# Optimization experiments

Hardware: AMD Instinct MI355X
Metric: run time of the kernel (lower is better)

The kernel has to match this reference:

```python
import jax, jax.numpy as jnp
import numpy as np

BATCH, IN, HID, OUT = 8192, 784, 4096, 10


def setup_inputs() -> dict:
    key = jax.random.key(0)
    k_x, k_w1, k_b1, k_w2, k_b2 = jax.random.split(key, 5)
    return {
        "x": jax.random.normal(k_x, (BATCH, IN), dtype=jnp.float32),
        "W1": jax.random.normal(k_w1, (HID, IN), dtype=jnp.float32) * 0.05,
        "b1": jax.random.normal(k_b1, (HID,), dtype=jnp.float32) * 0.05,
        "W2": jax.random.normal(k_w2, (OUT, HID), dtype=jnp.float32) * 0.05,
        "b2": jax.random.normal(k_b2, (OUT,), dtype=jnp.float32) * 0.05,
    }


def reference(x, W1, b1, W2, b2):
    # x: [B, 784] -- first layer, so the input is NOT binarized (BNN convention
    # for in_features == 784); only the weight is sign-quantized.
    x = x.reshape(-1, IN)
    Wb1 = jnp.sign(W1)                       # binarized weights in {-1, 0, +1}
    h = jnp.einsum("bi,hi->bh", x, Wb1) + b1  # BinarizeLinear fc1
    h = jnp.clip(h, -1.0, 1.0)               # Hardtanh
    out = jnp.einsum("bh,oh->bo", h, W2) + b2  # plain float fc2
    return out
```

## Files before the change

kernel.cpp:

```cpp
#include <hip/hip_runtime.h>
#include <cstdint>


#define BATCH 8192
#define IN_F  784
#define HID   4096
#define OUT_F 10
#define KP    832
#define NKT   13
#define BM    256
#define BN    256
#define BK    64
#define NCT   (HID / BN)
#define HCS   264

typedef unsigned short u16;
typedef __attribute__((ext_vector_type(4))) unsigned short u16x4;
typedef __attribute__((ext_vector_type(8)))  _Float16 f16x8;
typedef __attribute__((ext_vector_type(4)))  float    f32x4;
typedef __attribute__((ext_vector_type(16))) float    f32x16;

#define BARRIER() do { asm volatile("" ::: "memory"); \
                       __builtin_amdgcn_s_barrier();  \
                       asm volatile("" ::: "memory"); } while (0)
#define WAITV(n)  asm volatile("s_waitcnt vmcnt(" #n ")" ::: "memory")
#define WAITL0()  asm volatile("s_waitcnt lgkmcnt(0)" ::: "memory")

__device__ __forceinline__ u16 f2h(float f) {
  union { _Float16 h; u16 u; } c;
  c.h = (_Float16)f;
  return c.u;
}

__device__ __forceinline__ void gl_lds16(const void* g, void* l) {
  __builtin_amdgcn_global_load_lds(
      (const __attribute__((address_space(1))) uint32_t*)g,
      (__attribute__((address_space(3))) uint32_t*)l, 16, 0, 0);
}

__global__ void prep_kernel(const float* __restrict__ x, const float* __restrict__ W1,
                            const float* __restrict__ W2,
                            u16* __restrict__ xh, u16* __restrict__ wh,
                            u16* __restrict__ w2h) {
  const int stride = gridDim.x * blockDim.x;
  const int gid = blockIdx.x * blockDim.x + threadIdx.x;
  const int KP4 = KP / 4;
  const int IN4 = IN_F / 4;
  const float4* x4 = (const float4*)x;
  const float4* w4 = (const float4*)W1;
  for (int i = gid; i < BATCH * KP4; i += stride) {
    int b = i / KP4, k = i - b * KP4;
    u16x4 o = {0, 0, 0, 0};
    if (k < IN4) {
      float4 v = x4[(size_t)b * IN4 + k];
      o[0] = f2h(v.x); o[1] = f2h(v.y); o[2] = f2h(v.z); o[3] = f2h(v.w);
    }
    *(u16x4*)&xh[(size_t)b * KP + k * 4] = o;
  }
  for (int i = gid; i < HID * KP4; i += stride) {
    int h = i / KP4, k = i - h * KP4;
    u16x4 o = {0, 0, 0, 0};
    if (k < IN4) {
      float4 v = w4[(size_t)h * IN4 + k];
      o[0] = v.x > 0.f ? 0x3C00 : (v.x < 0.f ? 0xBC00 : 0);
      o[1] = v.y > 0.f ? 0x3C00 : (v.y < 0.f ? 0xBC00 : 0);
      o[2] = v.z > 0.f ? 0x3C00 : (v.z < 0.f ? 0xBC00 : 0);
      o[3] = v.w > 0.f ? 0x3C00 : (v.w < 0.f ? 0xBC00 : 0);
    }
    *(u16x4*)&wh[(size_t)h * KP + k * 4] = o;
  }
  for (int i = gid; i < 16 * HID; i += stride) {
    int o = i >> 12, k = i & (HID - 1);
    w2h[i] = (o < OUT_F) ? f2h(W2[o * HID + k]) : (u16)0;
  }
}

__global__ void __launch_bounds__(512, 2) gemm_kernel(
    const u16* __restrict__ xh, const u16* __restrict__ wh,
    const u16* __restrict__ w2h, const float* __restrict__ b1,
    float* __restrict__ part) {
  __shared__ union {
    struct { u16 A[2][BM * BK]; u16 B[2][BN * BK]; } m;
    struct { u16 hc[128 * HCS]; u16 w2[16 * 256]; } e;
  } sm;

  const int t   = threadIdx.x;
  const int ct  = blockIdx.x;
  const int br  = blockIdx.y;
  const int w   = t >> 6;
  const int l   = t & 63;
  const int wm  = w >> 2;
  const int wn  = w & 3;
  const int lo  = l & 31;
  const int hi  = l >> 5;
  const int g   = l >> 4;
  const int r16 = l & 15;

  const int  srow  = t >> 3;
  const int  sslot = (t & 7) ^ (srow & 7);
  const u16* gA = xh + (size_t)(br * BM) * KP + sslot * 8;
  const u16* gB = wh + (size_t)(ct * BN) * KP + sslot * 8;

  auto stage = [&](int tile) {
    const int b = tile & 1;
#pragma unroll
    for (int c = 0; c < 4; ++c)
      gl_lds16(gA + (size_t)(c * 64 + srow) * KP + tile * BK,
               &sm.m.A[b][c * 4096 + t * 8]);
#pragma unroll
    for (int c = 0; c < 4; ++c)
      gl_lds16(gB + (size_t)(c * 64 + srow) * KP + tile * BK,
               &sm.m.B[b][c * 4096 + t * 8]);
  };
  auto rdA = [&](int p, int mi, int kk) -> f16x8 {
    int row = mi * 64 + wm * 32 + lo;
    return *(const f16x8*)&sm.m.A[p][row * 64 + (((kk * 2 + hi) ^ (row & 7)) << 3)];
  };
  auto rdB = [&](int p, int nh, int kk) -> f16x8 {
    int row = nh * 128 + wn * 32 + lo;
    return *(const f16x8*)&sm.m.B[p][row * 64 + (((kk * 2 + hi) ^ (row & 7)) << 3)];
  };

  f32x16 acc[4][2] = {};
  f16x8 af[2][4], bf[2][2];

#define RD(S, P, KK) do {                                             \
    _Pragma("unroll") for (int mi_ = 0; mi_ < 4; ++mi_) af[S][mi_] = rdA(P, mi_, KK); \
    _Pragma("unroll") for (int nh_ = 0; nh_ < 2; ++nh_) bf[S][nh_] = rdB(P, nh_, KK); \
  } while (0)
#define MFMA8(S) do {                                                 \
    __builtin_amdgcn_s_setprio(1);                                    \
    _Pragma("unroll") for (int mi_ = 0; mi_ < 4; ++mi_)               \
      _Pragma("unroll") for (int nh_ = 0; nh_ < 2; ++nh_)             \
        acc[mi_][nh_] = __builtin_amdgcn_mfma_f32_32x32x16_f16(       \
            af[S][mi_], bf[S][nh_], acc[mi_][nh_], 0, 0, 0);          \
    __builtin_amdgcn_s_setprio(0);                                    \
  } while (0)

  stage(0);
  WAITV(0);
  BARRIER();
  RD(0, 0, 0);

  for (int tt = 0; tt < NKT; ++tt) {
    const int  p    = tt & 1;
    const bool more = (tt + 1 < NKT);
    if (more) stage(tt + 1);
    RD(1, p, 1);  MFMA8(0);
    RD(0, p, 2);  MFMA8(1);
    RD(1, p, 3);  MFMA8(0);
    if (more) {
      WAITL0();
      WAITV(0);
      BARRIER();
      RD(0, p ^ 1, 0);
    }
    MFMA8(1);
  }

  WAITL0();
  BARRIER();
  {
    int row = t >> 5, sp = t & 31;
    int ls = (sp & 24) | ((sp ^ row) & 7);
    gl_lds16(w2h + (size_t)row * HID + ct * BN + ls * 8, &sm.e.w2[t * 8]);
  }
  float b1v[2];
#pragma unroll
  for (int nh = 0; nh < 2; ++nh) b1v[nh] = b1[ct * BN + nh * 128 + wn * 32 + lo];

  float* partBase = part + ((size_t)ct * BATCH + br * BM) * 16;

#pragma unroll
  for (int p = 0; p < 2; ++p) {
    if (p == 1) BARRIER();
#pragma unroll
    for (int mi = 0; mi < 2; ++mi)
#pragma unroll
      for (int nh = 0; nh < 2; ++nh)
#pragma unroll
        for (int r = 0; r < 16; ++r) {
          float v = acc[p * 2 + mi][nh][r] + b1v[nh];
          v = fminf(fmaxf(v, -1.f), 1.f);
          int crow = (r & 3) + 8 * (r >> 2) + 4 * hi;
          sm.e.hc[(mi * 64 + wm * 32 + crow) * HCS + nh * 128 + wn * 32 + lo] = f2h(v);
        }
    if (p == 0) { WAITV(0); }
    BARRIER();
    f32x4 acc2 = {};
#pragma unroll
    for (int kk = 0; kk < 8; ++kk) {
      f16x8 a2 = *(const f16x8*)&sm.e.hc[(w * 16 + r16) * HCS + kk * 32 + g * 8];
      int s   = kk * 4 + g;
      int sp2 = (s & 24) | ((s ^ r16) & 7);
      f16x8 b2f = *(const f16x8*)&sm.e.w2[r16 * 256 + sp2 * 8];
      acc2 = __builtin_amdgcn_mfma_f32_16x16x32_f16(a2, b2f, acc2, 0, 0, 0);
    }
#pragma unroll
    for (int r = 0; r < 4; ++r)
      partBase[(size_t)(p * 128 + w * 16 + g * 4 + r) * 16 + r16] = acc2[r];
  }
}

__global__ void reduce_kernel(const float* __restrict__ part, const float* __restrict__ b2,
                              float* __restrict__ out) {
  int i = blockIdx.x * blockDim.x + threadIdx.x;
  if (i >= BATCH * OUT_F) return;
  int b = i / OUT_F, o = i - b * OUT_F;
  float acc = b2[o];
#pragma unroll
  for (int c = 0; c < NCT; ++c)
    acc += part[((size_t)c * BATCH + b) * 16 + o];
  out[i] = acc;
}

extern "C" void kernel_launch(void* const* d_in, const int* in_sizes, int n_in,
                              void* d_out, int out_size, void* d_ws, size_t ws_size,
                              hipStream_t stream) {
  const float* x  = (const float*)d_in[0];
  const float* W1 = (const float*)d_in[1];
  const float* b1 = (const float*)d_in[2];
  const float* W2 = (const float*)d_in[3];
  const float* b2 = (const float*)d_in[4];
  float* out = (float*)d_out;

  u16* xh  = (u16*)d_ws;
  u16* wh  = xh + (size_t)BATCH * KP;
  u16* w2h = wh + (size_t)HID * KP;
  float* part = (float*)(w2h + 16 * HID);

  hipLaunchKernelGGL(prep_kernel, dim3(2048), dim3(256), 0, stream, x, W1, W2, xh, wh, w2h);
  hipLaunchKernelGGL(gemm_kernel, dim3(NCT, BATCH / BM), dim3(512), 0, stream,
                     xh, wh, w2h, b1, part);
  hipLaunchKernelGGL(reduce_kernel, dim3((BATCH * OUT_F + 255) / 256), dim3(256), 0, stream,
                     part, b2, out);
}
```

Baseline: 67.26 us.

## Switch main GEMM to 16x16x32 MFMA with split staging and barrier-phased schedule

Replaces the 32x32x16 MFMA tiling with 16x16x32 MFMAs, giving each wave an interleaved 8x4 grid of 16x16 accumulators. The next-tile global-to-LDS loads are split into four half-chunks, and each chunk is issued between the four MFMA phases of a K-tile, with barriers and sched_barrier fencing every phase. The goal is to spread load issue across the compute and keep MFMA pipes fed. The cost is many more barriers per tile, and fragments are no longer double-buffered in registers, so LDS read latency is exposed at each phase.

```diff
diff --git a/kernel.cpp b/kernel.cpp
--- a/kernel.cpp
+++ b/kernel.cpp
@@ -18,13 +18,13 @@
 typedef __attribute__((ext_vector_type(4))) unsigned short u16x4;
 typedef __attribute__((ext_vector_type(8)))  _Float16 f16x8;
 typedef __attribute__((ext_vector_type(4)))  float    f32x4;
-typedef __attribute__((ext_vector_type(16))) float    f32x16;
 
 #define BARRIER() do { asm volatile("" ::: "memory"); \
                        __builtin_amdgcn_s_barrier();  \
                        asm volatile("" ::: "memory"); } while (0)
 #define WAITV(n)  asm volatile("s_waitcnt vmcnt(" #n ")" ::: "memory")
-#define WAITL0()  asm volatile("s_waitcnt lgkmcnt(0)" ::: "memory")
+#define WAITL0()  do { asm volatile("s_waitcnt lgkmcnt(0)" ::: "memory"); \
+                       __builtin_amdgcn_sched_barrier(0); } while (0)
 
 __device__ __forceinline__ u16 f2h(float f) {
   union { _Float16 h; u16 u; } c;
@@ -91,71 +91,95 @@
   const int l   = t & 63;
   const int wm  = w >> 2;
   const int wn  = w & 3;
-  const int lo  = l & 31;
-  const int hi  = l >> 5;
   const int g   = l >> 4;
   const int r16 = l & 15;
+  const int swz = (r16 & 7) << 3;
 
   const int  srow  = t >> 3;
   const int  sslot = (t & 7) ^ (srow & 7);
   const u16* gA = xh + (size_t)(br * BM) * KP + sslot * 8;
   const u16* gB = wh + (size_t)(ct * BN) * KP + sslot * 8;
 
-  auto stage = [&](int tile) {
+  auto stA2 = [&](int tile, int h) {
     const int b = tile & 1;
 #pragma unroll
-    for (int c = 0; c < 4; ++c)
+    for (int c = 2 * h; c < 2 * h + 2; ++c)
       gl_lds16(gA + (size_t)(c * 64 + srow) * KP + tile * BK,
                &sm.m.A[b][c * 4096 + t * 8]);
-#pragma unroll
-    for (int c = 0; c < 4; ++c)
+  };
+  auto stB2 = [&](int tile, int h) {
+    const int b = tile & 1;
+#pragma unroll
+    for (int c = 2 * h; c < 2 * h + 2; ++c)
       gl_lds16(gB + (size_t)(c * 64 + srow) * KP + tile * BK,
                &sm.m.B[b][c * 4096 + t * 8]);
   };
-  auto rdA = [&](int p, int mi, int kk) -> f16x8 {
-    int row = mi * 64 + wm * 32 + lo;
-    return *(const f16x8*)&sm.m.A[p][row * 64 + (((kk * 2 + hi) ^ (row & 7)) << 3)];
-  };
-  auto rdB = [&](int p, int nh, int kk) -> f16x8 {
-    int row = nh * 128 + wn * 32 + lo;
-    return *(const f16x8*)&sm.m.B[p][row * 64 + (((kk * 2 + hi) ^ (row & 7)) << 3)];
-  };
-
-  f32x16 acc[4][2] = {};
-  f16x8 af[2][4], bf[2][2];
-
-#define RD(S, P, KK) do {                                             \
-    _Pragma("unroll") for (int mi_ = 0; mi_ < 4; ++mi_) af[S][mi_] = rdA(P, mi_, KK); \
-    _Pragma("unroll") for (int nh_ = 0; nh_ < 2; ++nh_) bf[S][nh_] = rdB(P, nh_, KK); \
-  } while (0)
-#define MFMA8(S) do {                                                 \
+  auto rdA = [&](int p, int MI, int kk) -> f16x8 {
+    int row = MI * 32 + wm * 16 + r16;
+    return *(const f16x8*)&sm.m.A[p][row * 64 + ((kk * 32 + g * 8) ^ swz)];
+  };
+  auto rdB = [&](int p, int nj, int kk) -> f16x8 {
+    int row = wn * 64 + nj * 16 + r16;
+    return *(const f16x8*)&sm.m.B[p][row * 64 + ((kk * 32 + g * 8) ^ swz)];
+  };
+
+  f32x4 acc[8][4] = {};
+  f16x8 af[4], bf0[4], bf1[4];
+
+#define MFMA16(MH, BF) do {                                           \
     __builtin_amdgcn_s_setprio(1);                                    \
     _Pragma("unroll") for (int mi_ = 0; mi_ < 4; ++mi_)               \
-      _Pragma("unroll") for (int nh_ = 0; nh_ < 2; ++nh_)             \
-        acc[mi_][nh_] = __builtin_amdgcn_mfma_f32_32x32x16_f16(       \
-            af[S][mi_], bf[S][nh_], acc[mi_][nh_], 0, 0, 0);          \
+      _Pragma("unroll") for (int nj_ = 0; nj_ < 4; ++nj_)             \
+        acc[(MH) * 4 + mi_][nj_] = __builtin_amdgcn_mfma_f32_16x16x32_f16( \
+            af[mi_], BF[nj_], acc[(MH) * 4 + mi_][nj_], 0, 0, 0);     \
     __builtin_amdgcn_s_setprio(0);                                    \
   } while (0)
 
-  stage(0);
-  WAITV(0);
+  stA2(0, 0); stB2(0, 0); stB2(0, 1); stA2(0, 1);
+  WAITV(2);
   BARRIER();
-  RD(0, 0, 0);
 
   for (int tt = 0; tt < NKT; ++tt) {
     const int  p    = tt & 1;
     const bool more = (tt + 1 < NKT);
-    if (more) stage(tt + 1);
-    RD(1, p, 1);  MFMA8(0);
-    RD(0, p, 2);  MFMA8(1);
-    RD(1, p, 3);  MFMA8(0);
-    if (more) {
-      WAITL0();
-      WAITV(0);
-      BARRIER();
-      RD(0, p ^ 1, 0);
-    }
-    MFMA8(1);
+
+#pragma unroll
+    for (int mi = 0; mi < 4; ++mi) af[mi] = rdA(p, mi, 0);
+#pragma unroll
+    for (int nj = 0; nj < 4; ++nj) bf0[nj] = rdB(p, nj, 0);
+    if (more) stA2(tt + 1, 0);
+    BARRIER();
+    WAITL0();
+    MFMA16(0, bf0);
+    if (more) { WAITV(2); } else { WAITV(0); }
+    BARRIER();
+
+#pragma unroll
+    for (int mi = 0; mi < 4; ++mi) af[mi] = rdA(p, 4 + mi, 0);
+    if (more) stB2(tt + 1, 0);
+    BARRIER();
+    WAITL0();
+    MFMA16(1, bf0);
+    BARRIER();
+
+#pragma unroll
+    for (int mi = 0; mi < 4; ++mi) af[mi] = rdA(p, mi, 1);
+#pragma unroll
+    for (int nj = 0; nj < 4; ++nj) bf1[nj] = rdB(p, nj, 1);
+    if (more) stB2(tt + 1, 1);
+    BARRIER();
+    WAITL0();
+    MFMA16(0, bf1);
+    BARRIER();
+
+#pragma unroll
+    for (int mi = 0; mi < 4; ++mi) af[mi] = rdA(p, 4 + mi, 1);
+    if (more) stA2(tt + 1, 1);
+    BARRIER();
+    WAITL0();
+    MFMA16(1, bf1);
+    if (more) WAITV(2);
+    BARRIER();
   }
 
   WAITL0();
@@ -165,9 +189,9 @@
     int ls = (sp & 24) | ((sp ^ row) & 7);
     gl_lds16(w2h + (size_t)row * HID + ct * BN + ls * 8, &sm.e.w2[t * 8]);
   }
-  float b1v[2];
-#pragma unroll
-  for (int nh = 0; nh < 2; ++nh) b1v[nh] = b1[ct * BN + nh * 128 + wn * 32 + lo];
+  float b1v[4];
+#pragma unroll
+  for (int ni = 0; ni < 4; ++ni) b1v[ni] = b1[ct * BN + wn * 64 + ni * 16 + r16];
 
   float* partBase = part + ((size_t)ct * BATCH + br * BM) * 16;
 
@@ -175,15 +199,14 @@
   for (int p = 0; p < 2; ++p) {
     if (p == 1) BARRIER();
 #pragma unroll
-    for (int mi = 0; mi < 2; ++mi)
-#pragma unroll
-      for (int nh = 0; nh < 2; ++nh)
-#pragma unroll
-        for (int r = 0; r < 16; ++r) {
-          float v = acc[p * 2 + mi][nh][r] + b1v[nh];
+    for (int mi = 0; mi < 4; ++mi)
+#pragma unroll
+      for (int ni = 0; ni < 4; ++ni)
+#pragma unroll
+        for (int r = 0; r < 4; ++r) {
+          float v = acc[p * 4 + mi][ni][r] + b1v[ni];
           v = fminf(fmaxf(v, -1.f), 1.f);
-          int crow = (r & 3) + 8 * (r >> 2) + 4 * hi;
-          sm.e.hc[(mi * 64 + wm * 32 + crow) * HCS + nh * 128 + wn * 32 + lo] = f2h(v);
+          sm.e.hc[(mi * 32 + wm * 16 + g * 4 + r) * HCS + wn * 64 + ni * 16 + r16] = f2h(v);
         }
     if (p == 0) { WAITV(0); }
     BARRIER();
```

Result: faster. 65.79 us (-2.2%).
